# Optimization experiments

Hardware: AMD Instinct MI355X
Metric: run time of the kernel (lower is better)

Reference implementation:

```python
import jax, jax.numpy as jnp
import numpy as np

# Model dims (match init_kwargs)
H = 16        # num query heads
HKV = 4       # num key/value heads
D = 128       # head dim
HID = H * D   # hidden size = 2048
W = 4         # ring world size; we simulate rank W-1 (sees all kv shards)
SL = 2048     # local (per-rank) sequence length


def _block_attn(q, kb, vb, scale, causal):
    # q: [B,H,Sl,D], kb/vb: [B,H,Sl,D]
    S = jnp.einsum('bhqd,bhkd->bhqk', q, kb) * scale
    if causal:
        mask = jnp.triu(jnp.ones((q.shape[2], kb.shape[2]), dtype=bool), k=1)
        S = jnp.where(mask[None, None], -jnp.inf, S)
    S_max = jnp.max(S, axis=-1, keepdims=True)
    exp_S = jnp.exp(S - S_max)
    exp_sum = jnp.sum(exp_S, axis=-1, keepdims=True)
    lse = jnp.log(exp_sum) + S_max            # [B,H,Sl,1]
    O = jnp.einsum('bhqk,bhkd->bhqd', exp_S / exp_sum, vb)
    return O, lse


def _ring_attention_fwd(x_q, x_kv, Wq, Wk, Wv, Wo):
    B, Sl, hid = x_q.shape
    n_rep = H // HKV
    scale = 1.0 / np.sqrt(D).astype(np.float32)

    q = (x_q @ Wq.T).reshape(B, Sl, H, D).transpose(0, 2, 1, 3)          # [B,H,Sl,D]
    k = (x_kv @ Wk.T).reshape(B, -1, HKV, D).transpose(0, 2, 1, 3)       # [B,Hkv,Stot,D]
    v = (x_kv @ Wv.T).reshape(B, -1, HKV, D).transpose(0, 2, 1, 3)
    # repeat_kv (GQA)
    k = jnp.repeat(k, n_rep, axis=1)                                     # [B,H,Stot,D]
    v = jnp.repeat(v, n_rep, axis=1)
    # split kv into W ring shards along sequence
    kb = k.reshape(B, H, W, Sl, D)
    vb = v.reshape(B, H, W, Sl, D)

    out, lse = None, None
    rank = W - 1
    for step in range(W):  # fixed small ring loop
        blk = rank - step  # shard held at this ring step (own shard first)
        bo, blse = _block_attn(q, kb[:, :, blk], vb[:, :, blk], scale, causal=(step == 0))
        if out is None:
            out, lse = bo, blse
        else:
            # online merge (matches update_out_and_lse)
            out = out - jax.nn.sigmoid(blse - lse) * (out - bo)
            lse = lse - jax.nn.log_sigmoid(lse - blse)

    out = out.transpose(0, 2, 1, 3).reshape(B, Sl, H * D)
    return out @ Wo.T


def setup_inputs() -> dict:
    key = jax.random.key(0)
    ks = jax.random.split(key, 6)
    s = 0.02
    return {
        'x_q': jax.random.normal(ks[0], (1, SL, HID), dtype=jnp.float32),
        'x_kv': jax.random.normal(ks[1], (1, W * SL, HID), dtype=jnp.float32),
        'Wq': jax.random.normal(ks[2], (HID, HID), dtype=jnp.float32) * s,
        'Wk': jax.random.normal(ks[3], (HKV * D, HID), dtype=jnp.float32) * s,
        'Wv': jax.random.normal(ks[4], (HKV * D, HID), dtype=jnp.float32) * s,
        'Wo': jax.random.normal(ks[5], (HID, HID), dtype=jnp.float32) * s,
    }


def reference(x_q, x_kv, Wq, Wk, Wv, Wo):
    return _ring_attention_fwd(x_q, x_kv, Wq, Wk, Wv, Wo)
```

## Files before the change

kernel.cpp:

```cpp
#include <hip/hip_runtime.h>
#include <stdint.h>

typedef unsigned short u16;
typedef short bf16x8 __attribute__((ext_vector_type(8)));
typedef float f32x4 __attribute__((ext_vector_type(4)));
typedef float f32x16 __attribute__((ext_vector_type(16)));

#define MFMA16(a, b, c) __builtin_amdgcn_mfma_f32_16x16x32_bf16(a, b, c, 0, 0, 0)
#define MFMA32(a, b, c) __builtin_amdgcn_mfma_f32_32x32x16_bf16(a, b, c, 0, 0, 0)

__device__ __forceinline__ void ld_lds16(const void* g, void* l) {
  __builtin_amdgcn_global_load_lds(
      (const __attribute__((address_space(1))) void*)(uint64_t)(uintptr_t)g,
      (__attribute__((address_space(3))) void*)(uint32_t)(uintptr_t)l,
      16, 0, 0);
}

__device__ __forceinline__ u16 f32_to_bf16(float f) {
  uint32_t u = __float_as_uint(f);
  return (u16)((u + 0x7FFFu + ((u >> 16) & 1u)) >> 16);
}

__device__ __forceinline__ uint32_t cvt_pk_bf16(float a, float b) {
  uint32_t r;
  asm("v_cvt_pk_bf16_f32 %0, %1, %2" : "=v"(r) : "v"(a), "v"(b));
  return r;
}

__device__ __forceinline__ void perm_swap(uint32_t& x, uint32_t& y) {
  asm volatile("v_permlane32_swap_b32 %0, %1" : "+v"(x), "+v"(y));
}

__global__ void cvt_all(const float* __restrict__ xq, const float* __restrict__ xkv,
                        const float* __restrict__ Wq, const float* __restrict__ Wk,
                        const float* __restrict__ Wv, const float* __restrict__ Wo,
                        u16* __restrict__ xq_b, u16* __restrict__ xkv_b,
                        u16* __restrict__ wq_b, u16* __restrict__ wk_b,
                        u16* __restrict__ wv_b, u16* __restrict__ wo_b) {
  const int M4 = 1 << 20;
  const int total = 7 * M4 + (M4 >> 1);
  int i = blockIdx.x * blockDim.x + threadIdx.x;
  int stride = gridDim.x * blockDim.x;
  for (; i < total; i += stride) {
    const float* src;
    u16* dst;
    int off;
    if (i < M4)                         { src = xq;  dst = xq_b;  off = i; }
    else if (i < 5 * M4)                { src = xkv; dst = xkv_b; off = i - M4; }
    else if (i < 6 * M4)                { src = Wq;  dst = wq_b;  off = i - 5 * M4; }
    else if (i < 6 * M4 + (M4 >> 2))    { src = Wk;  dst = wk_b;  off = i - 6 * M4; }
    else if (i < 6 * M4 + (M4 >> 1))    { src = Wv;  dst = wv_b;  off = i - 6 * M4 - (M4 >> 2); }
    else                                { src = Wo;  dst = wo_b;  off = i - 6 * M4 - (M4 >> 1); }
    float4 v = reinterpret_cast<const float4*>(src)[off];
    ushort4 o;
    o.x = f32_to_bf16(v.x); o.y = f32_to_bf16(v.y);
    o.z = f32_to_bf16(v.z); o.w = f32_to_bf16(v.w);
    reinterpret_cast<ushort4*>(dst)[off] = o;
  }
}

__device__ __forceinline__ void gemm_body(const u16* __restrict__ A,
                                          const u16* __restrict__ B,
                                          void* __restrict__ Cv, int M, int N,
                                          int K, float alpha, int bx, int by,
                                          int outf32, u16* lA, u16* lB) {
  const int tid = threadIdx.x;
  const int lane = tid & 63;
  const int w = tid >> 6;
  const int c = lane & 15, g = lane >> 4;
  const int wm = (w & 1) * 64, wn = (w >> 1) * 32;
  const int m0 = by * 128, n0 = bx * 64;
  const int sr = tid >> 3, sc = tid & 7;

  f32x4 acc[4][2] = {};

  for (int k0 = 0; k0 < K; k0 += 64) {
    __syncthreads();
#pragma unroll
    for (int p = 0; p < 4; ++p) {
      int row = p * 32 + sr;
      int gc = sc ^ (row & 7);
      ld_lds16(A + (size_t)(m0 + row) * K + k0 + gc * 8, &lA[row * 64 + sc * 8]);
    }
#pragma unroll
    for (int p = 0; p < 2; ++p) {
      int idx = p * 256 + tid;
      int row = idx >> 3, cc = idx & 7;
      int gc = cc ^ (row & 7);
      ld_lds16(B + (size_t)(n0 + row) * K + k0 + gc * 8, &lB[row * 64 + cc * 8]);
    }
    __syncthreads();
#pragma unroll
    for (int kc = 0; kc < 2; ++kc) {
      bf16x8 a[4], b[2];
#pragma unroll
      for (int t = 0; t < 4; ++t) {
        int row = wm + t * 16 + c;
        int ch = (g + 4 * kc) ^ (row & 7);
        a[t] = *(const bf16x8*)&lA[row * 64 + ch * 8];
      }
#pragma unroll
      for (int t = 0; t < 2; ++t) {
        int row = wn + t * 16 + c;
        int ch = (g + 4 * kc) ^ (row & 7);
        b[t] = *(const bf16x8*)&lB[row * 64 + ch * 8];
      }
#pragma unroll
      for (int i = 0; i < 4; ++i)
#pragma unroll
        for (int j = 0; j < 2; ++j)
          acc[i][j] = MFMA16(a[i], b[j], acc[i][j]);
    }
  }

#pragma unroll
  for (int i = 0; i < 4; ++i)
#pragma unroll
    for (int j = 0; j < 2; ++j)
#pragma unroll
      for (int r = 0; r < 4; ++r) {
        int mm = m0 + wm + i * 16 + g * 4 + r;
        int nn = n0 + wn + j * 16 + c;
        float v = acc[i][j][r] * alpha;
        if (outf32)
          ((float*)Cv)[(size_t)mm * N + nn] = v;
        else
          ((u16*)Cv)[(size_t)mm * N + nn] = f32_to_bf16(v);
      }
}

__global__ __launch_bounds__(256, 4)
void gemm3(const u16* __restrict__ xq_b, const u16* __restrict__ wq_b,
           u16* __restrict__ Qb, const u16* __restrict__ xkv_b,
           const u16* __restrict__ wk_b, u16* __restrict__ Kb,
           const u16* __restrict__ wv_b, u16* __restrict__ VTb, float qscale) {
  __shared__ u16 lA[128 * 64];
  __shared__ u16 lB[64 * 64];
  int b = blockIdx.x;
  if (b < 512) {
    gemm_body(xq_b, wq_b, Qb, 2048, 2048, 2048, qscale, b & 31, b >> 5, 0, lA, lB);
  } else if (b < 1024) {
    b -= 512;
    gemm_body(xkv_b, wk_b, Kb, 8192, 512, 2048, 1.0f, b & 7, b >> 3, 0, lA, lB);
  } else {
    b -= 1024;
    gemm_body(wv_b, xkv_b, VTb, 512, 8192, 2048, 1.0f, b & 127, b >> 7, 0, lA, lB);
  }
}

__global__ __launch_bounds__(256, 4)
void gemm_out(const u16* __restrict__ A, const u16* __restrict__ B,
              float* __restrict__ Cv) {
  __shared__ u16 lA[128 * 64];
  __shared__ u16 lB[64 * 64];
  gemm_body(A, B, Cv, 2048, 2048, 2048, 1.0f, blockIdx.x, blockIdx.y, 1, lA, lB);
}

__global__ __launch_bounds__(256, 2)
void attn_kernel(const u16* __restrict__ Q, const u16* __restrict__ Kg,
                 const u16* __restrict__ VT, float* __restrict__ Opart,
                 float* __restrict__ mlp) {
  __shared__ u16 lK[2][64 * 128];
  __shared__ u16 lV[2][128 * 64];

  const int tid = threadIdx.x;
  const int w = tid >> 6, lane = tid & 63;
  const int ql = lane & 31, hi = lane >> 5;
  const int bx = blockIdx.x;
  const int h = bx & 15, kvs = bx >> 8;
  const int qbr = (bx >> 4) & 15;
  const int qb = kvs ? qbr : 15 - qbr;
  const int hk = h >> 2;
  const int i0 = qb * 128;
  const int q0 = i0 + w * 32;

  const int nt = ((i0 + 6271) >> 6) + 1;
  const int nth = nt >> 1;
  const int t0 = kvs ? nth : 0;
  const int ntt = (kvs ? nt : nth) - t0;
  const int tsafe = (i0 + 6081) >> 6;
  int nmain = tsafe + 1 - t0;
  if (nmain > ntt) nmain = ntt;
  if (nmain < 0) nmain = 0;

  bf16x8 qf[8];
#pragma unroll
  for (int kc = 0; kc < 8; ++kc)
    qf[kc] = *(const bf16x8*)&Q[(size_t)(q0 + ql) * 2048 + h * 128 + kc * 16 + hi * 8];

  bf16x8 onesB;
#pragma unroll
  for (int i = 0; i < 8; ++i) onesB[i] = (short)0x3F80;

  f32x16 a[4] = {};
  f32x16 lacc = {};

  auto stage = [&](int buf, int t) {
    const int j0 = t << 6;
#pragma unroll
    for (int p = 0; p < 4; ++p) {
      int idx = p * 256 + tid;
      int row = idx >> 4, cc = idx & 15;
      int gc = cc ^ (row & 15);
      ld_lds16(Kg + (size_t)(j0 + row) * 512 + hk * 128 + gc * 8,
               &lK[buf][row * 128 + cc * 8]);
    }
#pragma unroll
    for (int p = 0; p < 4; ++p) {
      int idx = p * 256 + tid;
      int row = idx >> 3, cc = idx & 7;
      int gc = cc ^ (row & 7);
      ld_lds16(VT + (size_t)(hk * 128 + row) * 8192 + j0 + gc * 8,
               &lV[buf][row * 64 + cc * 8]);
    }
  };

  auto finish = [&](f32x16& sv, bf16x8& pA, bf16x8& pB) {
#pragma unroll
    for (int r = 0; r < 16; ++r) sv[r] = __builtin_amdgcn_exp2f(sv[r]);
    uint32_t A0 = cvt_pk_bf16(sv[0], sv[1]);
    uint32_t B0 = cvt_pk_bf16(sv[4], sv[5]);
    perm_swap(A0, B0);
    uint32_t A1 = cvt_pk_bf16(sv[2], sv[3]);
    uint32_t B1 = cvt_pk_bf16(sv[6], sv[7]);
    perm_swap(A1, B1);
    uint32_t A2 = cvt_pk_bf16(sv[8], sv[9]);
    uint32_t B2 = cvt_pk_bf16(sv[12], sv[13]);
    perm_swap(A2, B2);
    uint32_t A3 = cvt_pk_bf16(sv[10], sv[11]);
    uint32_t B3 = cvt_pk_bf16(sv[14], sv[15]);
    perm_swap(A3, B3);
    union { uint32_t u[4]; bf16x8 v; } pa, pb;
    pa.u[0] = A0; pa.u[1] = A1; pa.u[2] = B0; pa.u[3] = B1;
    pb.u[0] = A2; pb.u[1] = A3; pb.u[2] = B2; pb.u[3] = B3;
    pA = pa.v;
    pB = pb.v;
  };

  stage(0, t0);

  int it = 0;
  auto run_tiles = [&](int end, bool domask) {
    for (; it < end; ++it) {
      const int curb = it & 1;
      const int j0 = (t0 + it) << 6;
      if (it + 1 < ntt) {
        stage(curb ^ 1, t0 + it + 1);
        asm volatile("s_waitcnt vmcnt(8)" ::: "memory");
      } else {
        asm volatile("s_waitcnt vmcnt(0)" ::: "memory");
      }
      __builtin_amdgcn_s_barrier();

      f32x16 s0 = {}, s1 = {};
      bf16x8 pbf[4];
      __builtin_amdgcn_s_setprio(1);
#pragma unroll
      for (int kc = 0; kc < 8; ++kc) {
        int ch = kc * 2 + hi;
        bf16x8 kfa = *(const bf16x8*)&lK[curb][ql * 128 + (ch ^ (ql & 15)) * 8];
        s0 = MFMA32(kfa, qf[kc], s0);
      }
      __builtin_amdgcn_s_setprio(0);
#pragma unroll
      for (int kc = 0; kc < 8; ++kc) {
        int ch = kc * 2 + hi;
        bf16x8 kfb = *(const bf16x8*)&lK[curb][(32 + ql) * 128 + (ch ^ (ql & 15)) * 8];
        s1 = MFMA32(kfb, qf[kc], s1);
      }
      if (domask) {
#pragma unroll
        for (int r = 0; r < 16; ++r) {
          int jrow = (r & 3) + 8 * (r >> 2) + 4 * hi;
          if (j0 + jrow > q0 + ql + 6144) s0[r] = -1e30f;
        }
      }
      finish(s0, pbf[0], pbf[1]);
      lacc = MFMA32(pbf[0], onesB, lacc);
      lacc = MFMA32(pbf[1], onesB, lacc);
#pragma unroll
      for (int kc = 0; kc < 2; ++kc)
#pragma unroll
        for (int dt = 0; dt < 4; ++dt) {
          int row = dt * 32 + ql;
          int ch = (kc * 2 + hi) ^ (row & 7);
          bf16x8 vf = *(const bf16x8*)&lV[curb][row * 64 + ch * 8];
          a[dt] = MFMA32(pbf[kc], vf, a[dt]);
        }
      if (domask) {
#pragma unroll
        for (int r = 0; r < 16; ++r) {
          int jrow = (r & 3) + 8 * (r >> 2) + 4 * hi;
          if (j0 + 32 + jrow > q0 + ql + 6144) s1[r] = -1e30f;
        }
      }
      finish(s1, pbf[2], pbf[3]);
      __builtin_amdgcn_s_setprio(1);
      lacc = MFMA32(pbf[2], onesB, lacc);
      lacc = MFMA32(pbf[3], onesB, lacc);
#pragma unroll
      for (int kc = 2; kc < 4; ++kc)
#pragma unroll
        for (int dt = 0; dt < 4; ++dt) {
          int row = dt * 32 + ql;
          int ch = (kc * 2 + hi) ^ (row & 7);
          bf16x8 vf = *(const bf16x8*)&lV[curb][row * 64 + ch * 8];
          a[dt] = MFMA32(pbf[kc], vf, a[dt]);
        }
      __builtin_amdgcn_s_setprio(0);

      __builtin_amdgcn_s_barrier();
    }
  };

  run_tiles(nmain, false);
  run_tiles(ntt, true);

  const size_t pbase = ((size_t)(kvs * 16 + h) * 16 + qb);
  float* Op = Opart + pbase * 16384;
  float* mlb = mlp + pbase * 256;
#pragma unroll
  for (int dt = 0; dt < 4; ++dt)
#pragma unroll
    for (int r = 0; r < 16; ++r) {
      int qrow = w * 32 + (r & 3) + 8 * (r >> 2) + 4 * hi;
      Op[(size_t)qrow * 128 + dt * 32 + ql] = a[dt][r];
    }
  if (ql == 0) {
#pragma unroll
    for (int r = 0; r < 16; ++r)
      mlb[128 + w * 32 + (r & 3) + 8 * (r >> 2) + 4 * hi] = lacc[r];
  }
}

__global__ __launch_bounds__(256)
void attn_merge(const float* __restrict__ Opart, const float* __restrict__ mlp,
                u16* __restrict__ O) {
  const int bx = blockIdx.x;
  const int h = bx >> 4, qb = bx & 15;
  const int q = threadIdx.x & 127, hf = threadIdx.x >> 7;
  const size_t p0 = ((size_t)(0 + h) * 16 + qb);
  const size_t p1 = ((size_t)(16 + h) * 16 + qb);
  float ll0 = mlp[p0 * 256 + 128 + q], ll1 = mlp[p1 * 256 + 128 + q];
  float inv = 1.f / (ll0 + ll1);
  const float* A = Opart + p0 * 16384 + (size_t)q * 128 + hf * 64;
  const float* B = Opart + p1 * 16384 + (size_t)q * 128 + hf * 64;
  u16* out = O + (size_t)(qb * 128 + q) * 2048 + h * 128 + hf * 64;
#pragma unroll
  for (int d = 0; d < 64; d += 4) {
    float4 a = *(const float4*)&A[d];
    float4 b = *(const float4*)&B[d];
    ushort4 o;
    o.x = f32_to_bf16((a.x + b.x) * inv);
    o.y = f32_to_bf16((a.y + b.y) * inv);
    o.z = f32_to_bf16((a.z + b.z) * inv);
    o.w = f32_to_bf16((a.w + b.w) * inv);
    *(ushort4*)&out[d] = o;
  }
}

extern "C" void kernel_launch(void* const* d_in, const int* in_sizes, int n_in,
                              void* d_out, int out_size, void* d_ws, size_t ws_size,
                              hipStream_t stream) {
  (void)in_sizes; (void)n_in; (void)out_size; (void)ws_size;
  const float* xq = (const float*)d_in[0];
  const float* xkv = (const float*)d_in[1];
  const float* Wq = (const float*)d_in[2];
  const float* Wk = (const float*)d_in[3];
  const float* Wv = (const float*)d_in[4];
  const float* Wo = (const float*)d_in[5];

  u16* ws = (u16*)d_ws;
  const size_t M1 = 1024 * 1024;
  u16* xq_b  = ws;
  u16* xkv_b = ws + 4 * M1;
  u16* wq_b  = ws + 20 * M1;
  u16* wk_b  = ws + 24 * M1;
  u16* wv_b  = ws + 25 * M1;
  u16* wo_b  = ws + 26 * M1;
  u16* Qb    = ws + 30 * M1;
  u16* Kb    = ws + 34 * M1;
  u16* VTb   = ws + 38 * M1;
  u16* Ob    = ws + 42 * M1;
  float* Opart = (float*)d_ws;
  float* mlptr = Opart + 8388608;

  cvt_all<<<2048, 256, 0, stream>>>(xq, xkv, Wq, Wk, Wv, Wo,
                                    xq_b, xkv_b, wq_b, wk_b, wv_b, wo_b);

  gemm3<<<1536, 256, 0, stream>>>(xq_b, wq_b, Qb, xkv_b, wk_b, Kb, wv_b, VTb,
                                  0.12752837f);

  attn_kernel<<<512, 256, 0, stream>>>(Qb, Kb, VTb, Opart, mlptr);
  attn_merge<<<256, 256, 0, stream>>>(Opart, mlptr, Ob);

  gemm_out<<<dim3(32, 16), 256, 0, stream>>>(Ob, wo_b, (float*)d_out);
}
```

Measured before the change: 275.2 us.

## Split attention KV range three ways and single-buffer V to fit three blocks per CU

The attention kernel now splits each query block's KV tiles into three contiguous chunks instead of two, launching 768 blocks instead of 512. The merge kernel sums three partial outputs and row sums. To let three blocks sit on one CU, the V tile in LDS drops from double to single buffering, and launch bounds rise to 3. The loop is reordered so V for the current tile loads right after the top barrier and overlaps the QK MFMAs, with a second barrier before PV. This adds an extra barrier and a partial-output write per split, and exposes some V load latency, in exchange for better CU fill and occupancy.

```diff
diff --git a/kernel.cpp b/kernel.cpp
--- a/kernel.cpp
+++ b/kernel.cpp
@@ -156,12 +156,12 @@
   gemm_body(A, B, Cv, 2048, 2048, 2048, 1.0f, blockIdx.x, blockIdx.y, 1, lA, lB);
 }
 
-__global__ __launch_bounds__(256, 2)
+__global__ __launch_bounds__(256, 3)
 void attn_kernel(const u16* __restrict__ Q, const u16* __restrict__ Kg,
                  const u16* __restrict__ VT, float* __restrict__ Opart,
                  float* __restrict__ mlp) {
   __shared__ u16 lK[2][64 * 128];
-  __shared__ u16 lV[2][128 * 64];
+  __shared__ u16 lV[128 * 64];
 
   const int tid = threadIdx.x;
   const int w = tid >> 6, lane = tid & 63;
@@ -169,15 +169,15 @@
   const int bx = blockIdx.x;
   const int h = bx & 15, kvs = bx >> 8;
   const int qbr = (bx >> 4) & 15;
-  const int qb = kvs ? qbr : 15 - qbr;
+  const int qb = 15 - qbr;
   const int hk = h >> 2;
   const int i0 = qb * 128;
   const int q0 = i0 + w * 32;
 
   const int nt = ((i0 + 6271) >> 6) + 1;
-  const int nth = nt >> 1;
-  const int t0 = kvs ? nth : 0;
-  const int ntt = (kvs ? nt : nth) - t0;
+  const int t0 = (nt * kvs) / 3;
+  const int t1 = (nt * (kvs + 1)) / 3;
+  const int ntt = t1 - t0;
   const int tsafe = (i0 + 6081) >> 6;
   int nmain = tsafe + 1 - t0;
   if (nmain > ntt) nmain = ntt;
@@ -195,7 +195,7 @@
   f32x16 a[4] = {};
   f32x16 lacc = {};
 
-  auto stage = [&](int buf, int t) {
+  auto stageK = [&](int buf, int t) {
     const int j0 = t << 6;
 #pragma unroll
     for (int p = 0; p < 4; ++p) {
@@ -205,13 +205,16 @@
       ld_lds16(Kg + (size_t)(j0 + row) * 512 + hk * 128 + gc * 8,
                &lK[buf][row * 128 + cc * 8]);
     }
+  };
+  auto stageV = [&](int t) {
+    const int j0 = t << 6;
 #pragma unroll
     for (int p = 0; p < 4; ++p) {
       int idx = p * 256 + tid;
       int row = idx >> 3, cc = idx & 7;
       int gc = cc ^ (row & 7);
       ld_lds16(VT + (size_t)(hk * 128 + row) * 8192 + j0 + gc * 8,
-               &lV[buf][row * 64 + cc * 8]);
+               &lV[row * 64 + cc * 8]);
     }
   };
 
@@ -237,20 +240,17 @@
     pB = pb.v;
   };
 
-  stage(0, t0);
+  stageK(0, t0);
 
   int it = 0;
   auto run_tiles = [&](int end, bool domask) {
     for (; it < end; ++it) {
       const int curb = it & 1;
       const int j0 = (t0 + it) << 6;
-      if (it + 1 < ntt) {
-        stage(curb ^ 1, t0 + it + 1);
-        asm volatile("s_waitcnt vmcnt(8)" ::: "memory");
-      } else {
-        asm volatile("s_waitcnt vmcnt(0)" ::: "memory");
-      }
+      asm volatile("s_waitcnt vmcnt(0)" ::: "memory");
       __builtin_amdgcn_s_barrier();
+      stageV(t0 + it);
+      if (it + 1 < ntt) stageK(curb ^ 1, t0 + it + 1);
 
       f32x16 s0 = {}, s1 = {};
       bf16x8 pbf[4];
@@ -276,6 +276,11 @@
         }
       }
       finish(s0, pbf[0], pbf[1]);
+      if (it + 1 < ntt)
+        asm volatile("s_waitcnt vmcnt(4)" ::: "memory");
+      else
+        asm volatile("s_waitcnt vmcnt(0)" ::: "memory");
+      __builtin_amdgcn_s_barrier();
       lacc = MFMA32(pbf[0], onesB, lacc);
       lacc = MFMA32(pbf[1], onesB, lacc);
 #pragma unroll
@@ -284,7 +289,7 @@
         for (int dt = 0; dt < 4; ++dt) {
           int row = dt * 32 + ql;
           int ch = (kc * 2 + hi) ^ (row & 7);
-          bf16x8 vf = *(const bf16x8*)&lV[curb][row * 64 + ch * 8];
+          bf16x8 vf = *(const bf16x8*)&lV[row * 64 + ch * 8];
           a[dt] = MFMA32(pbf[kc], vf, a[dt]);
         }
       if (domask) {
@@ -304,12 +309,10 @@
         for (int dt = 0; dt < 4; ++dt) {
           int row = dt * 32 + ql;
           int ch = (kc * 2 + hi) ^ (row & 7);
-          bf16x8 vf = *(const bf16x8*)&lV[curb][row * 64 + ch * 8];
+          bf16x8 vf = *(const bf16x8*)&lV[row * 64 + ch * 8];
           a[dt] = MFMA32(pbf[kc], vf, a[dt]);
         }
       __builtin_amdgcn_s_setprio(0);
-
-      __builtin_amdgcn_s_barrier();
     }
   };
 
@@ -339,22 +342,30 @@
   const int bx = blockIdx.x;
   const int h = bx >> 4, qb = bx & 15;
   const int q = threadIdx.x & 127, hf = threadIdx.x >> 7;
-  const size_t p0 = ((size_t)(0 + h) * 16 + qb);
-  const size_t p1 = ((size_t)(16 + h) * 16 + qb);
-  float ll0 = mlp[p0 * 256 + 128 + q], ll1 = mlp[p1 * 256 + 128 + q];
-  float inv = 1.f / (ll0 + ll1);
-  const float* A = Opart + p0 * 16384 + (size_t)q * 128 + hf * 64;
-  const float* B = Opart + p1 * 16384 + (size_t)q * 128 + hf * 64;
+
+  float lsum = 0.f;
+#pragma unroll
+  for (int s = 0; s < 3; ++s) {
+    size_t pidx = ((size_t)(s * 16 + h) * 16 + qb);
+    lsum += mlp[pidx * 256 + 128 + q];
+  }
+  float inv = 1.f / lsum;
+
   u16* out = O + (size_t)(qb * 128 + q) * 2048 + h * 128 + hf * 64;
 #pragma unroll
   for (int d = 0; d < 64; d += 4) {
-    float4 a = *(const float4*)&A[d];
-    float4 b = *(const float4*)&B[d];
+    float acc0 = 0.f, acc1 = 0.f, acc2 = 0.f, acc3 = 0.f;
+#pragma unroll
+    for (int s = 0; s < 3; ++s) {
+      size_t pidx = ((size_t)(s * 16 + h) * 16 + qb);
+      float4 v = *(const float4*)&Opart[pidx * 16384 + (size_t)q * 128 + hf * 64 + d];
+      acc0 += v.x; acc1 += v.y; acc2 += v.z; acc3 += v.w;
+    }
     ushort4 o;
-    o.x = f32_to_bf16((a.x + b.x) * inv);
-    o.y = f32_to_bf16((a.y + b.y) * inv);
-    o.z = f32_to_bf16((a.z + b.z) * inv);
-    o.w = f32_to_bf16((a.w + b.w) * inv);
+    o.x = f32_to_bf16(acc0 * inv);
+    o.y = f32_to_bf16(acc1 * inv);
+    o.z = f32_to_bf16(acc2 * inv);
+    o.w = f32_to_bf16(acc3 * inv);
     *(ushort4*)&out[d] = o;
   }
 }
@@ -383,7 +394,7 @@
   u16* VTb   = ws + 38 * M1;
   u16* Ob    = ws + 42 * M1;
   float* Opart = (float*)d_ws;
-  float* mlptr = Opart + 8388608;
+  float* mlptr = Opart + 12582912;
 
   cvt_all<<<2048, 256, 0, stream>>>(xq, xkv, Wq, Wk, Wv, Wo,
                                     xq_b, xkv_b, wq_b, wk_b, wv_b, wo_b);
@@ -391,7 +402,7 @@
   gemm3<<<1536, 256, 0, stream>>>(xq_b, wq_b, Qb, xkv_b, wk_b, Kb, wv_b, VTb,
                                   0.12752837f);
 
-  attn_kernel<<<512, 256, 0, stream>>>(Qb, Kb, VTb, Opart, mlptr);
+  attn_kernel<<<768, 256, 0, stream>>>(Qb, Kb, VTb, Opart, mlptr);
   attn_merge<<<256, 256, 0, stream>>>(Opart, mlptr, Ob);
 
   gemm_out<<<dim3(32, 16), 256, 0, stream>>>(Ob, wo_b, (float*)d_out);
```

New measurement: 638.6 us. 132% more time.
